# Performance work log

Hardware: AMD Instinct MI355X
Metric: run time of the kernel (lower is better)

The kernel has to match this reference:

```python
import jax, jax.numpy as jnp
import numpy as np

IN_CH, OUT_CH, K, STRIDE, PAD = 256, 256, 5, 1, 2


def setup_inputs() -> dict:
    key = jax.random.key(0)
    kx, kw = jax.random.split(key)
    x = jax.random.normal(kx, (32, IN_CH, 4096), dtype=jnp.float32)
    # kaiming_uniform_(a=sqrt(5)) -> bound = 1/sqrt(fan_in), fan_in = in_ch*k
    bound = 1.0 / np.sqrt(IN_CH * K)
    weight = jax.random.uniform(kw, (OUT_CH, IN_CH, K), dtype=jnp.float32,
                                minval=-bound, maxval=bound)
    bias = jnp.zeros((OUT_CH,), dtype=jnp.float32)
    return {"x": x, "weight": weight, "bias": bias}


def reference(x, weight, bias):
    # x: [B, C_in, W]; weight: [C_out, C_in, K] -> out: [B, C_out, W_out]
    out = jax.lax.conv_general_dilated(
        x, weight,
        window_strides=(STRIDE,),
        padding=[(PAD, PAD)],
        dimension_numbers=("NCH", "OIH", "NCH"),
    )
    return out + bias[None, :, None]
```

## Files before the change

### kernel.cpp

```cpp
#include <hip/hip_runtime.h>
#include <hip/hip_bf16.h>

typedef unsigned short u16;
typedef unsigned int u32;
typedef unsigned long long u64;
typedef __attribute__((ext_vector_type(8))) short short8;
typedef __attribute__((ext_vector_type(4))) float floatx4;

#define NB 32
#define NCI 256
#define NCO 256
#define NW 4096
#define NK 5

#define W3ROWB 80
#define W3TILE (256 * W3ROWB)
#define W3_BYTES (40 * W3TILE)

#define XROWB 80
#define XROWS 264
#define XBUF (XROWS * XROWB)


__global__ void wprep(const float* __restrict__ wgt, u16* __restrict__ W3) {
    int i = blockIdx.x * 256 + threadIdx.x;
    if (i >= NCO * NCI * NK) return;
    int k  = i % NK;
    int ci = (i / NK) % NCI;
    int co = i / (NCI * NK);
    int cb = ci >> 5, cr = ci & 31;
    __hip_bfloat16 h = __float2bfloat16(wgt[i]);
    W3[((size_t)(cb * NK + k) * 256 + co) * 40 + cr] = *reinterpret_cast<u16*>(&h);
}

__device__ __forceinline__ u16 bf16bits(float f) {
    __hip_bfloat16 h = __float2bfloat16(f);
    return *reinterpret_cast<u16*>(&h);
}


__global__ __launch_bounds__(512, 2)
void conv_mfma(const float* __restrict__ x, const u16* __restrict__ W3,
               const float* __restrict__ bias, float* __restrict__ out) {
    __shared__ __align__(16) char xlds[2 * XBUF];

    const int bid  = blockIdx.x;
    const int wt   = bid & 15;
    const int b    = bid >> 4;
    const int tid  = threadIdx.x;
    const int lane = tid & 63;
    const int wave = tid >> 6;
    const int wm   = wave >> 2;
    const int wn   = wave & 3;
    const int mrow = lane & 15;
    const int g    = lane >> 4;
    const int w0   = wt * 256;

    floatx4 acc[8][4];
#pragma unroll
    for (int mi = 0; mi < 8; ++mi)
#pragma unroll
        for (int ni = 0; ni < 4; ++ni)
            acc[mi][ni] = (floatx4){0.f, 0.f, 0.f, 0.f};

    const float* xb = x + (size_t)b * NCI * NW;

    const int h  = tid >> 8;
    const int wi = tid & 255;

    const int hside = tid >> 5;
    const int hr    = (tid >> 3) & 3;
    const int hcq   = tid & 7;
    const int hrow  = hside ? (260 + hr) : hr;
    const int hwg   = hside ? (w0 + 256 + hr) : (w0 - 4 + hr);
    const bool hvalid = (hwg >= 0) && (hwg < NW);

    {
        float va[8], vb[8];
        float hv[4] = {0.f, 0.f, 0.f, 0.f};
#pragma unroll
        for (int it = 0; it < 8; ++it) {
            int ci0 = it * 4 + h * 2;
            va[it] = xb[(size_t)ci0 * NW + w0 + wi];
            vb[it] = xb[(size_t)(ci0 + 1) * NW + w0 + wi];
        }
        if (tid < 64 && hvalid)
#pragma unroll
            for (int q = 0; q < 4; ++q)
                hv[q] = xb[(size_t)(hcq * 4 + q) * NW + hwg];

#pragma unroll
        for (int it = 0; it < 8; ++it) {
            u32 p = (u32)bf16bits(va[it]) | ((u32)bf16bits(vb[it]) << 16);
            *(u32*)(xlds + (wi + 4) * XROWB + (it * 4 + h * 2) * 2) = p;
        }
        if (tid < 64) {
            u64 p = (u64)bf16bits(hv[0]) | ((u64)bf16bits(hv[1]) << 16) |
                    ((u64)bf16bits(hv[2]) << 32) | ((u64)bf16bits(hv[3]) << 48);
            *(u64*)(xlds + hrow * XROWB + hcq * 8) = p;
        }
    }
    __syncthreads();

    for (int cb = 0; cb < 8; ++cb) {
        const char* cur = xlds + (cb & 1) * XBUF;
        char* nxt       = xlds + ((cb + 1) & 1) * XBUF;
        const bool more = (cb < 7);

        float va[8], vb[8];
        float hv[4] = {0.f, 0.f, 0.f, 0.f};
        if (more) {
            const float* xcb = xb + (size_t)((cb + 1) * 32) * NW;
#pragma unroll
            for (int it = 0; it < 8; ++it) {
                int ci0 = it * 4 + h * 2;
                va[it] = xcb[(size_t)ci0 * NW + w0 + wi];
                vb[it] = xcb[(size_t)(ci0 + 1) * NW + w0 + wi];
            }
            if (tid < 64 && hvalid)
#pragma unroll
                for (int q = 0; q < 4; ++q)
                    hv[q] = xcb[(size_t)(hcq * 4 + q) * NW + hwg];
        }

#pragma unroll
        for (int t = 0; t < NK; ++t) {
            const char* wtile = (const char*)W3 + (size_t)(cb * NK + t) * W3TILE;
            short8 af[8], bf[4];
#pragma unroll
            for (int mi = 0; mi < 8; ++mi)
                af[mi] = *(const short8*)(wtile +
                         (wm * 128 + mi * 16 + mrow) * W3ROWB + g * 16);
#pragma unroll
            for (int ni = 0; ni < 4; ++ni)
                bf[ni] = *(const short8*)(cur +
                         (wn * 64 + ni * 16 + mrow + t + 2) * XROWB + g * 16);

            __builtin_amdgcn_s_setprio(1);
#pragma unroll
            for (int mi = 0; mi < 8; ++mi)
#pragma unroll
                for (int ni = 0; ni < 4; ++ni)
                    acc[mi][ni] = __builtin_amdgcn_mfma_f32_16x16x32_bf16(
                        af[mi], bf[ni], acc[mi][ni], 0, 0, 0);
            __builtin_amdgcn_s_setprio(0);
        }

        if (more) {
#pragma unroll
            for (int it = 0; it < 8; ++it) {
                u32 p = (u32)bf16bits(va[it]) | ((u32)bf16bits(vb[it]) << 16);
                *(u32*)(nxt + (wi + 4) * XROWB + (it * 4 + h * 2) * 2) = p;
            }
            if (tid < 64) {
                u64 p = (u64)bf16bits(hv[0]) | ((u64)bf16bits(hv[1]) << 16) |
                        ((u64)bf16bits(hv[2]) << 32) | ((u64)bf16bits(hv[3]) << 48);
                *(u64*)(nxt + hrow * XROWB + hcq * 8) = p;
            }
            __syncthreads();
        }
    }

#pragma unroll
    for (int mi = 0; mi < 8; ++mi) {
        int cobase = wm * 128 + mi * 16 + g * 4;
        float bv[4];
#pragma unroll
        for (int r = 0; r < 4; ++r) bv[r] = bias[cobase + r];
#pragma unroll
        for (int ni = 0; ni < 4; ++ni) {
            int col = w0 + wn * 64 + ni * 16 + mrow;
#pragma unroll
            for (int r = 0; r < 4; ++r)
                out[((size_t)b * NCO + cobase + r) * NW + col] =
                    acc[mi][ni][r] + bv[r];
        }
    }
}


__global__ void conv_naive(const float* __restrict__ x, const float* __restrict__ wgt,
                           const float* __restrict__ bias, float* __restrict__ out) {
    int w  = blockIdx.x * 256 + threadIdx.x;
    int co = blockIdx.y;
    int b  = blockIdx.z;
    float acc = bias[co];
    for (int ci = 0; ci < NCI; ci++) {
        const float* xr = x + ((size_t)b * NCI + ci) * NW;
        const float* wr = wgt + ((size_t)co * NCI + ci) * NK;
#pragma unroll
        for (int k = 0; k < NK; k++) {
            int wi = w + k - 2;
            if (wi >= 0 && wi < NW) acc += xr[wi] * wr[k];
        }
    }
    out[((size_t)b * NCO + co) * NW + w] = acc;
}


extern "C" void kernel_launch(void* const* d_in, const int* in_sizes, int n_in,
                              void* d_out, int out_size, void* d_ws, size_t ws_size,
                              hipStream_t stream) {
    const float* x    = (const float*)d_in[0];
    const float* wgt  = (const float*)d_in[1];
    const float* bias = (const float*)d_in[2];
    float* out        = (float*)d_out;

    if (ws_size < (size_t)W3_BYTES) {
        conv_naive<<<dim3(NW / 256, NCO, NB), 256, 0, stream>>>(x, wgt, bias, out);
        return;
    }

    u16* W3 = (u16*)d_ws;
    wprep<<<(NCO * NCI * NK + 255) / 256, 256, 0, stream>>>(wgt, W3);
    conv_mfma<<<512, 512, 0, stream>>>(x, W3, bias, out);
}
```

Baseline: 108.1 us.

## Halve conv width tile, switch to XOR-swizzled 64B LDS rows, double occupancy

Each block now covers 128 output positions instead of 256 and launches 1024 blocks. The 8 waves are arranged 4x2, each holding a 64x64 accumulator tile instead of 128x64, which cuts register use and allows 4 blocks per CU. The padded 80-byte rows for LDS and the weight workspace become dense 64-byte rows, with an XOR swizzle on LDS to avoid bank conflicts. Staging uses one 16-byte LDS store per thread, and the s_setprio hints are dropped. In exchange each block has a smaller tile, so weights are re-read more often and there is more halo overhead per output.

```diff
diff --git a/kernel.cpp b/kernel.cpp
--- a/kernel.cpp
+++ b/kernel.cpp
@@ -3,7 +3,6 @@
 
 typedef unsigned short u16;
 typedef unsigned int u32;
-typedef unsigned long long u64;
 typedef __attribute__((ext_vector_type(8))) short short8;
 typedef __attribute__((ext_vector_type(4))) float floatx4;
 
@@ -13,16 +12,15 @@
 #define NW 4096
 #define NK 5
 
-#define W3ROWB 80
-#define W3TILE (256 * W3ROWB)
-#define W3_BYTES (40 * W3TILE)
-
-#define XROWB 80
-#define XROWS 264
+#define W2_BYTES (40 * 256 * 64)
+
+#define XROWB 64
+#define XROWS 136
 #define XBUF (XROWS * XROWB)
-
-
-__global__ void wprep(const float* __restrict__ wgt, u16* __restrict__ W3) {
+#define XSWZ(r) ((((r) >> 1) & 3) << 4)
+
+
+__global__ void wprep(const float* __restrict__ wgt, u16* __restrict__ W2) {
     int i = blockIdx.x * 256 + threadIdx.x;
     if (i >= NCO * NCI * NK) return;
     int k  = i % NK;
@@ -30,7 +28,7 @@
     int co = i / (NCI * NK);
     int cb = ci >> 5, cr = ci & 31;
     __hip_bfloat16 h = __float2bfloat16(wgt[i]);
-    W3[((size_t)(cb * NK + k) * 256 + co) * 40 + cr] = *reinterpret_cast<u16*>(&h);
+    W2[((size_t)(cb * NK + k) * 256 + co) * 32 + cr] = *reinterpret_cast<u16*>(&h);
 }
 
 __device__ __forceinline__ u16 bf16bits(float f) {
@@ -39,65 +37,62 @@
 }
 
 
-__global__ __launch_bounds__(512, 2)
-void conv_mfma(const float* __restrict__ x, const u16* __restrict__ W3,
+__global__ __launch_bounds__(512, 4)
+void conv_mfma(const float* __restrict__ x, const u16* __restrict__ W2,
                const float* __restrict__ bias, float* __restrict__ out) {
     __shared__ __align__(16) char xlds[2 * XBUF];
 
     const int bid  = blockIdx.x;
-    const int wt   = bid & 15;
-    const int b    = bid >> 4;
+    const int wt   = bid & 31;
+    const int b    = bid >> 5;
     const int tid  = threadIdx.x;
     const int lane = tid & 63;
     const int wave = tid >> 6;
-    const int wm   = wave >> 2;
-    const int wn   = wave & 3;
+    const int wm   = wave >> 1;
+    const int wn   = wave & 1;
     const int mrow = lane & 15;
     const int g    = lane >> 4;
-    const int w0   = wt * 256;
-
-    floatx4 acc[8][4];
-#pragma unroll
-    for (int mi = 0; mi < 8; ++mi)
+    const int w0   = wt * 128;
+
+    floatx4 acc[4][4];
+#pragma unroll
+    for (int mi = 0; mi < 4; ++mi)
 #pragma unroll
         for (int ni = 0; ni < 4; ++ni)
             acc[mi][ni] = (floatx4){0.f, 0.f, 0.f, 0.f};
 
     const float* xb = x + (size_t)b * NCI * NW;
 
-    const int h  = tid >> 8;
-    const int wi = tid & 255;
-
-    const int hside = tid >> 5;
-    const int hr    = (tid >> 3) & 3;
-    const int hcq   = tid & 7;
-    const int hrow  = hside ? (260 + hr) : hr;
-    const int hwg   = hside ? (w0 + 256 + hr) : (w0 - 4 + hr);
-    const bool hvalid = (hwg >= 0) && (hwg < NW);
+    const int wloc = tid & 127;
+    const int q    = tid >> 7;
+    const int soff = (4 + wloc) * XROWB + ((q * 16) ^ XSWZ(4 + wloc));
+    const float* xcol = xb + (size_t)(q * 8) * NW + w0 + wloc;
+
+    const int hidx = tid >> 2;
+    const int hq   = tid & 3;
+    const int hr   = (hidx < 2) ? (2 + hidx) : (130 + hidx);
+    const int hw   = w0 + ((hidx < 2) ? (hidx - 2) : (126 + hidx));
+    const bool hok = (tid < 16) && (hw >= 0) && (hw < NW);
+    const int hoff = hr * XROWB + ((hq * 16) ^ XSWZ(hr));
 
     {
-        float va[8], vb[8];
-        float hv[4] = {0.f, 0.f, 0.f, 0.f};
-#pragma unroll
-        for (int it = 0; it < 8; ++it) {
-            int ci0 = it * 4 + h * 2;
-            va[it] = xb[(size_t)ci0 * NW + w0 + wi];
-            vb[it] = xb[(size_t)(ci0 + 1) * NW + w0 + wi];
-        }
-        if (tid < 64 && hvalid)
-#pragma unroll
-            for (int q = 0; q < 4; ++q)
-                hv[q] = xb[(size_t)(hcq * 4 + q) * NW + hwg];
-
-#pragma unroll
-        for (int it = 0; it < 8; ++it) {
-            u32 p = (u32)bf16bits(va[it]) | ((u32)bf16bits(vb[it]) << 16);
-            *(u32*)(xlds + (wi + 4) * XROWB + (it * 4 + h * 2) * 2) = p;
-        }
-        if (tid < 64) {
-            u64 p = (u64)bf16bits(hv[0]) | ((u64)bf16bits(hv[1]) << 16) |
-                    ((u64)bf16bits(hv[2]) << 32) | ((u64)bf16bits(hv[3]) << 48);
-            *(u64*)(xlds + hrow * XROWB + hcq * 8) = p;
+        u32 p[4];
+#pragma unroll
+        for (int jp = 0; jp < 4; ++jp) {
+            float a0 = xcol[(size_t)(2 * jp) * NW];
+            float a1 = xcol[(size_t)(2 * jp + 1) * NW];
+            p[jp] = (u32)bf16bits(a0) | ((u32)bf16bits(a1) << 16);
+        }
+        *(int4*)(xlds + soff) = *(int4*)p;
+        if (tid < 16) {
+            u32 hp[4];
+#pragma unroll
+            for (int jp = 0; jp < 4; ++jp) {
+                float a0 = hok ? xb[(size_t)(hq * 8 + 2 * jp) * NW + hw] : 0.f;
+                float a1 = hok ? xb[(size_t)(hq * 8 + 2 * jp + 1) * NW + hw] : 0.f;
+                hp[jp] = (u32)bf16bits(a0) | ((u32)bf16bits(a1) << 16);
+            }
+            *(int4*)(xlds + hoff) = *(int4*)hp;
         }
     }
     __syncthreads();
@@ -107,63 +102,57 @@
         char* nxt       = xlds + ((cb + 1) & 1) * XBUF;
         const bool more = (cb < 7);
 
-        float va[8], vb[8];
-        float hv[4] = {0.f, 0.f, 0.f, 0.f};
+        u32 p[4], hp[4];
         if (more) {
-            const float* xcb = xb + (size_t)((cb + 1) * 32) * NW;
-#pragma unroll
-            for (int it = 0; it < 8; ++it) {
-                int ci0 = it * 4 + h * 2;
-                va[it] = xcb[(size_t)ci0 * NW + w0 + wi];
-                vb[it] = xcb[(size_t)(ci0 + 1) * NW + w0 + wi];
-            }
-            if (tid < 64 && hvalid)
-#pragma unroll
-                for (int q = 0; q < 4; ++q)
-                    hv[q] = xcb[(size_t)(hcq * 4 + q) * NW + hwg];
+            const float* s = xcol + (size_t)((cb + 1) * 32) * NW;
+#pragma unroll
+            for (int jp = 0; jp < 4; ++jp) {
+                float a0 = s[(size_t)(2 * jp) * NW];
+                float a1 = s[(size_t)(2 * jp + 1) * NW];
+                p[jp] = (u32)bf16bits(a0) | ((u32)bf16bits(a1) << 16);
+            }
+            if (tid < 16) {
+                const float* sh = xb + (size_t)((cb + 1) * 32 + hq * 8) * NW + hw;
+#pragma unroll
+                for (int jp = 0; jp < 4; ++jp) {
+                    float a0 = hok ? sh[(size_t)(2 * jp) * NW] : 0.f;
+                    float a1 = hok ? sh[(size_t)(2 * jp + 1) * NW] : 0.f;
+                    hp[jp] = (u32)bf16bits(a0) | ((u32)bf16bits(a1) << 16);
+                }
+            }
         }
 
 #pragma unroll
         for (int t = 0; t < NK; ++t) {
-            const char* wtile = (const char*)W3 + (size_t)(cb * NK + t) * W3TILE;
-            short8 af[8], bf[4];
-#pragma unroll
-            for (int mi = 0; mi < 8; ++mi)
-                af[mi] = *(const short8*)(wtile +
-                         (wm * 128 + mi * 16 + mrow) * W3ROWB + g * 16);
-#pragma unroll
-            for (int ni = 0; ni < 4; ++ni)
-                bf[ni] = *(const short8*)(cur +
-                         (wn * 64 + ni * 16 + mrow + t + 2) * XROWB + g * 16);
-
-            __builtin_amdgcn_s_setprio(1);
-#pragma unroll
-            for (int mi = 0; mi < 8; ++mi)
+            const char* wtile = (const char*)W2 +
+                ((size_t)(cb * NK + t) * 256 + wm * 64) * 64;
+            short8 af[4], bf[4];
+#pragma unroll
+            for (int mi = 0; mi < 4; ++mi)
+                af[mi] = *(const short8*)(wtile + (mi * 16 + mrow) * 64 + g * 16);
+#pragma unroll
+            for (int ni = 0; ni < 4; ++ni) {
+                int r = wn * 64 + ni * 16 + mrow + t + 2;
+                bf[ni] = *(const short8*)(cur + r * XROWB + ((g * 16) ^ XSWZ(r)));
+            }
+#pragma unroll
+            for (int mi = 0; mi < 4; ++mi)
 #pragma unroll
                 for (int ni = 0; ni < 4; ++ni)
                     acc[mi][ni] = __builtin_amdgcn_mfma_f32_16x16x32_bf16(
                         af[mi], bf[ni], acc[mi][ni], 0, 0, 0);
-            __builtin_amdgcn_s_setprio(0);
         }
 
         if (more) {
-#pragma unroll
-            for (int it = 0; it < 8; ++it) {
-                u32 p = (u32)bf16bits(va[it]) | ((u32)bf16bits(vb[it]) << 16);
-                *(u32*)(nxt + (wi + 4) * XROWB + (it * 4 + h * 2) * 2) = p;
-            }
-            if (tid < 64) {
-                u64 p = (u64)bf16bits(hv[0]) | ((u64)bf16bits(hv[1]) << 16) |
-                        ((u64)bf16bits(hv[2]) << 32) | ((u64)bf16bits(hv[3]) << 48);
-                *(u64*)(nxt + hrow * XROWB + hcq * 8) = p;
-            }
+            *(int4*)(nxt + soff) = *(int4*)p;
+            if (tid < 16) *(int4*)(nxt + hoff) = *(int4*)hp;
             __syncthreads();
         }
     }
 
 #pragma unroll
-    for (int mi = 0; mi < 8; ++mi) {
-        int cobase = wm * 128 + mi * 16 + g * 4;
+    for (int mi = 0; mi < 4; ++mi) {
+        int cobase = wm * 64 + mi * 16 + g * 4;
         float bv[4];
 #pragma unroll
         for (int r = 0; r < 4; ++r) bv[r] = bias[cobase + r];
@@ -206,12 +195,12 @@
     const float* bias = (const float*)d_in[2];
     float* out        = (float*)d_out;
 
-    if (ws_size < (size_t)W3_BYTES) {
+    if (ws_size < (size_t)W2_BYTES) {
         conv_naive<<<dim3(NW / 256, NCO, NB), 256, 0, stream>>>(x, wgt, bias, out);
         return;
     }
 
-    u16* W3 = (u16*)d_ws;
-    wprep<<<(NCO * NCI * NK + 255) / 256, 256, 0, stream>>>(wgt, W3);
-    conv_mfma<<<512, 512, 0, stream>>>(x, W3, bias, out);
-}
+    u16* W2 = (u16*)d_ws;
+    wprep<<<(NCO * NCI * NK + 255) / 256, 256, 0, stream>>>(wgt, W2);
+    conv_mfma<<<1024, 512, 0, stream>>>(x, W2, bias, out);
+}
```

Result: slower. 209.5 us (+93.9%).
